# Kernel tuning notes

Hardware: AMD Instinct MI355X
Metric: run time of the kernel (lower is better)

## Reference

```python
import jax, jax.numpy as jnp
import numpy as np

B, N, C, L, H = 8, 128, 64, 3, 128  # batch, objects, channels, eq-layers, message hidden
NEG_SLOPE = 0.01  # torch leaky_relu default


def setup_inputs() -> dict:
    key = jax.random.key(0)
    ks = jax.random.split(key, 10)
    def p(k, shape, fan):
        return jax.random.normal(k, shape, dtype=jnp.float32) * np.float32(np.sqrt(2.0 / fan))
    return {
        "x": jax.random.normal(ks[0], (B, N, N, C), dtype=jnp.float32),
        "mask": jnp.ones((B, N, N, 1), dtype=jnp.float32),
        # MessageNet per eq-layer: Linear(C->H), Linear(H->H), Linear(H->C), stacked over L layers
        "msg_w1": p(ks[1], (L, H, C), C + H),
        "msg_b1": jnp.zeros((L, H), jnp.float32),
        "msg_w2": p(ks[2], (L, H, H), H + H),
        "msg_b2": jnp.zeros((L, H), jnp.float32),
        "msg_w3": p(ks[3], (L, C, H), H + C),
        "msg_b3": jnp.zeros((L, C), jnp.float32),
        # Eq2to2 params: coefs (in_dim, out_dim, 15), bias, diag_bias
        "coefs": p(ks[4], (L, C, C, 15), C + C + 15),
        "bias": jnp.zeros((L, C), jnp.float32),
        "diag_bias": jnp.zeros((L, C), jnp.float32),
    }


def leaky(x):
    return jax.nn.leaky_relu(x, NEG_SLOPE)


def eops_2_to_2(x):
    # x: (B, m, m, C) -> ops: (B, C, 15, m, m); aggregation='sum'
    t = jnp.transpose(x, (0, 3, 1, 2))            # (B, C, m, m)
    m = t.shape[-1]
    eye = jnp.eye(m, dtype=t.dtype)
    diag = jnp.diagonal(t, axis1=-2, axis2=-1)    # (B, C, m)
    sum_diag = diag.sum(-1, keepdims=True)        # (B, C, 1)
    sum_rows = t.sum(-1)                          # (B, C, m)  sum over j
    sum_cols = t.sum(-2)                          # (B, C, m)  sum over i
    sum_all = t.sum((-2, -1))[..., None]          # (B, C, 1)
    de = lambda v: v[..., :, None] * eye          # diag_embed with broadcast
    shp = t.shape
    bc = lambda a: jnp.broadcast_to(a, shp)
    ops = [
        de(diag),                                 # 1  diag -> diag
        de(sum_diag),                             # 2  trace -> diag
        de(sum_rows),                             # 3  row sums -> diag
        de(sum_cols),                             # 4  col sums -> diag
        de(sum_all),                              # 5  total sum -> diag
        bc(sum_cols[..., :, None]),               # 6  col sums broadcast over j
        bc(sum_rows[..., :, None]),               # 7  row sums broadcast over j
        bc(sum_cols[..., None, :]),               # 8  col sums broadcast over i
        bc(sum_rows[..., None, :]),               # 9  row sums broadcast over i
        t,                                        # 10 identity
        jnp.swapaxes(t, -2, -1),                  # 11 transpose
        bc(diag[..., :, None]),                   # 12 diag broadcast over j
        bc(diag[..., None, :]),                   # 13 diag broadcast over i
        bc(sum_diag[..., :, None]),               # 14 trace broadcast everywhere
        bc(sum_all[..., :, None]),                # 15 total sum broadcast everywhere
    ]
    return jnp.stack(ops, axis=2)                 # (B, C, 15, m, m)


def reference(x, mask, msg_w1, msg_b1, msg_w2, msg_b2, msg_w3, msg_b3, coefs, bias, diag_bias):
    m = x.shape[1]
    eye = jnp.eye(m, dtype=x.dtype)[None, :, :, None]  # (1, m, m, 1)
    for l in range(L):
        # MessageNet: pointwise MLP over channels, activation after each linear, then mask
        h = leaky(jnp.einsum('nijc,hc->nijh', x, msg_w1[l]) + msg_b1[l])
        h = leaky(jnp.einsum('nijc,hc->nijh', h, msg_w2[l]) + msg_b2[l])
        h = leaky(jnp.einsum('nijc,hc->nijh', h, msg_w3[l]) + msg_b3[l])
        h = h * mask
        # Eq2to2
        ops = eops_2_to_2(h)                              # (B, C, 15, m, m)
        out = jnp.einsum('dsb,ndbij->nijs', coefs[l], ops)
        out = out + bias[l][None, None, None, :] + eye * diag_bias[l][None, None, None, :]
        out = leaky(out)
        x = out * mask
    return x
```

## Files before the change

### kernel.cpp

```cpp
#include <hip/hip_runtime.h>
#include <hip/hip_bf16.h>

#define BB 8
#define NN 128
#define CC 64
#define LL 3
#define HH 128
#define NEG 0.01f
#define NPOS (BB*NN*NN)

typedef __attribute__((ext_vector_type(8))) short shortx8;
typedef __attribute__((ext_vector_type(4))) float f32x4;

#define OFF_HHI   0L
#define OFF_RS2   4194304L
#define OFF_XN    8388608L
#define OFF_RS    12582912L
#define OFF_DG    12648448L
#define OFF_RCDH  12713984L
#define OFF_RCDL  12812288L
#define OFF_U     12911616L
#define OFF_V     12977152L
#define OFF_D     13042688L
#define OFF_SB    13108224L

__device__ __forceinline__ float leaky(float v) { return v >= 0.f ? v : NEG * v; }

__device__ __forceinline__ short f2bf(float f) {
    return (short)__bfloat16_as_ushort(__float2bfloat16(f));
}
__device__ __forceinline__ float bf2f(short s) {
    unsigned u = ((unsigned)(unsigned short)s) << 16;
    return __builtin_bit_cast(float, u);
}
__device__ __forceinline__ unsigned pkf(float a, float b) {
    return (unsigned)(unsigned short)f2bf(a) | ((unsigned)(unsigned short)f2bf(b) << 16);
}
__device__ __forceinline__ shortx8 cvt8(const float* p) {
    float4 f0 = *(const float4*)p, f1 = *(const float4*)(p + 4);
    shortx8 r;
    r[0]=f2bf(f0.x); r[1]=f2bf(f0.y); r[2]=f2bf(f0.z); r[3]=f2bf(f0.w);
    r[4]=f2bf(f1.x); r[5]=f2bf(f1.y); r[6]=f2bf(f1.z); r[7]=f2bf(f1.w);
    return r;
}

__global__ void prep_kernel(const float* __restrict__ w1, const float* __restrict__ w2,
                            const float* __restrict__ w3, const float* __restrict__ coefs,
                            float* __restrict__ ws) {
    long idx = (long)blockIdx.x * 256 + threadIdx.x;
    short* sb = (short*)(ws + OFF_SB);
    if (idx < 24576) {
        sb[idx] = f2bf(w1[idx]);
    } else if (idx < 73728) {
        sb[idx] = f2bf(w2[idx - 24576]);
    } else if (idx < 98304) {
        sb[idx] = f2bf(w3[idx - 73728]);
    } else if (idx < 110592) {
        long r = idx - 98304; int l = (int)(r / 4096); int q = (int)(r % 4096);
        int s = q >> 6, d = q & 63;
        float v = coefs[(((long)l*CC + d)*CC + s)*15 + 9];
        short hi = f2bf(v);
        sb[98304 + r]  = hi;
        sb[110592 + r] = f2bf(v - bf2f(hi));
    } else if (idx < 122880) {
        long r = idx - 110592; int l = (int)(r / 4096); int q = (int)(r % 4096);
        int s = q >> 6, d = q & 63;
        float v = coefs[(((long)l*CC + d)*CC + s)*15 + 10];
        short hi = f2bf(v);
        sb[122880 + r] = hi;
        sb[135168 + r] = f2bf(v - bf2f(hi));
    } else if (idx < 233472) {
        long r = idx - 122880;
        int l = (int)(r / 36864); int q = (int)(r % 36864);
        int o = q / 192, k = q % 192;
        int wo = o >> 6, s = o & 63, wk = k >> 6, d = k & 63;
        const int sel[3][3] = {{5,6,11},{7,8,12},{3,2,0}};
        float v = coefs[(((long)l*CC + d)*CC + s)*15 + sel[wo][wk]];
        short hi = f2bf(v);
        sb[147456 + r] = hi;
        sb[258048 + r] = f2bf(v - bf2f(hi));
    }
}

__global__ __launch_bounds__(256, 5) void mlp_kernel(
    const float* __restrict__ xf, const short* __restrict__ xb,
    const float* __restrict__ mask,
    const float* __restrict__ b1, const float* __restrict__ b2, const float* __restrict__ b3,
    const short* __restrict__ wb1, const short* __restrict__ wb2, const short* __restrict__ wb3,
    short* __restrict__ hout, float* __restrict__ rowsum2, float* __restrict__ diagOut)
{
    __shared__ __align__(16) char lds[32768];
    const int t = threadIdx.x;
    const int lane = t & 63;
    const int w = t >> 6;
    const int arow = lane & 15;
    const int kgrp = lane >> 4;
    const long pos0 = (long)blockIdx.x * 64;
    const int XT = 16384;

    {
        const int row = t >> 2, q = t & 3;
        const long off = (pos0 + row)*CC + q*16;
        shortx8 v0, v1;
        if (xb) { v0 = *(const shortx8*)(xb + off); v1 = *(const shortx8*)(xb + off + 8); }
        else    { v0 = cvt8(xf + off);              v1 = cvt8(xf + off + 8); }
        const int swz = (row & 7) << 4;
        *(shortx8*)(&lds[XT + row*128 + ((q*32)      ^ swz)]) = v0;
        *(shortx8*)(&lds[XT + row*128 + ((q*32 + 16) ^ swz)]) = v1;
    }
    __syncthreads();

    {
        f32x4 acc[2][4];
        #pragma unroll
        for (int of = 0; of < 2; ++of)
            #pragma unroll
            for (int pf = 0; pf < 4; ++pf) acc[of][pf] = (f32x4){0.f,0.f,0.f,0.f};
        #pragma unroll
        for (int kk = 0; kk < 2; ++kk) {
            shortx8 bx[4];
            #pragma unroll
            for (int pf = 0; pf < 4; ++pf) {
                const int p = pf*16 + arow;
                bx[pf] = *(const shortx8*)(&lds[XT + p*128 + ((kk*64 + kgrp*16) ^ ((p & 7) << 4))]);
            }
            #pragma unroll
            for (int of = 0; of < 2; ++of) {
                const shortx8 a = *(const shortx8*)(wb1 + (long)(w*32 + of*16 + arow)*CC + kk*32 + kgrp*8);
                #pragma unroll
                for (int pf = 0; pf < 4; ++pf)
                    acc[of][pf] = __builtin_amdgcn_mfma_f32_16x16x32_bf16(a, bx[pf], acc[of][pf], 0, 0, 0);
            }
        }
        #pragma unroll
        for (int of = 0; of < 2; ++of) {
            const int o0 = w*32 + of*16 + kgrp*4;
            const float4 bv = *(const float4*)(b1 + o0);
            #pragma unroll
            for (int pf = 0; pf < 4; ++pf) {
                const int p = pf*16 + arow;
                unsigned u0 = pkf(leaky(acc[of][pf][0] + bv.x), leaky(acc[of][pf][1] + bv.y));
                unsigned u1 = pkf(leaky(acc[of][pf][2] + bv.z), leaky(acc[of][pf][3] + bv.w));
                *(uint2*)(&lds[p*256 + ((o0*2) ^ ((p & 15) << 4))]) = make_uint2(u0, u1);
            }
        }
    }
    __syncthreads();

    {
        f32x4 acc[2][4];
        #pragma unroll
        for (int of = 0; of < 2; ++of)
            #pragma unroll
            for (int pf = 0; pf < 4; ++pf) acc[of][pf] = (f32x4){0.f,0.f,0.f,0.f};
        #pragma unroll
        for (int kk = 0; kk < 4; ++kk) {
            shortx8 bx[4];
            #pragma unroll
            for (int pf = 0; pf < 4; ++pf) {
                const int p = pf*16 + arow;
                bx[pf] = *(const shortx8*)(&lds[p*256 + ((kk*64 + kgrp*16) ^ ((p & 15) << 4))]);
            }
            #pragma unroll
            for (int of = 0; of < 2; ++of) {
                const shortx8 a = *(const shortx8*)(wb2 + (long)(w*32 + of*16 + arow)*HH + kk*32 + kgrp*8);
                #pragma unroll
                for (int pf = 0; pf < 4; ++pf)
                    acc[of][pf] = __builtin_amdgcn_mfma_f32_16x16x32_bf16(a, bx[pf], acc[of][pf], 0, 0, 0);
            }
        }
        __syncthreads();
        #pragma unroll
        for (int of = 0; of < 2; ++of) {
            const int o0 = w*32 + of*16 + kgrp*4;
            const float4 bv = *(const float4*)(b2 + o0);
            #pragma unroll
            for (int pf = 0; pf < 4; ++pf) {
                const int p = pf*16 + arow;
                unsigned u0 = pkf(leaky(acc[of][pf][0] + bv.x), leaky(acc[of][pf][1] + bv.y));
                unsigned u1 = pkf(leaky(acc[of][pf][2] + bv.z), leaky(acc[of][pf][3] + bv.w));
                *(uint2*)(&lds[16384 + p*256 + ((o0*2) ^ ((p & 15) << 4))]) = make_uint2(u0, u1);
            }
        }
    }
    __syncthreads();

    {
        f32x4 acc[4];
        #pragma unroll
        for (int pf = 0; pf < 4; ++pf) acc[pf] = (f32x4){0.f,0.f,0.f,0.f};
        #pragma unroll
        for (int kk = 0; kk < 4; ++kk) {
            const shortx8 a = *(const shortx8*)(wb3 + (long)(w*16 + arow)*HH + kk*32 + kgrp*8);
            #pragma unroll
            for (int pf = 0; pf < 4; ++pf) {
                const int p = pf*16 + arow;
                const shortx8 bx = *(const shortx8*)(&lds[16384 + p*256 + ((kk*64 + kgrp*16) ^ ((p & 15) << 4))]);
                acc[pf] = __builtin_amdgcn_mfma_f32_16x16x32_bf16(a, bx, acc[pf], 0, 0, 0);
            }
        }
        const int o0 = w*16 + kgrp*4;
        const float4 bv = *(const float4*)(b3 + o0);
        const int rowIdx = (int)(pos0 >> 7);
        const int half64 = (int)(pos0 & 127);
        const int pDiag  = (rowIdx & 127) - half64;
        float rs0 = 0.f, rs1 = 0.f, rs2 = 0.f, rs3 = 0.f;
        #pragma unroll
        for (int pf = 0; pf < 4; ++pf) {
            const int p = pf*16 + arow;
            const long pos = pos0 + p;
            const float mv = mask[pos];
            float v0 = leaky(acc[pf][0] + bv.x) * mv;
            float v1 = leaky(acc[pf][1] + bv.y) * mv;
            float v2 = leaky(acc[pf][2] + bv.z) * mv;
            float v3 = leaky(acc[pf][3] + bv.w) * mv;
            rs0 += v0; rs1 += v1; rs2 += v2; rs3 += v3;
            if (p == pDiag)
                *(float4*)(diagOut + (long)rowIdx*CC + o0) = make_float4(v0, v1, v2, v3);
            *(uint2*)(hout + pos*CC + o0) = make_uint2(pkf(v0, v1), pkf(v2, v3));
        }
        #pragma unroll
        for (int m = 1; m < 16; m <<= 1) {
            rs0 += __shfl_xor(rs0, m);
            rs1 += __shfl_xor(rs1, m);
            rs2 += __shfl_xor(rs2, m);
            rs3 += __shfl_xor(rs3, m);
        }
        if (arow == 0)
            *(float4*)(rowsum2 + (long)blockIdx.x*CC + o0) = make_float4(rs0, rs1, rs2, rs3);
    }
}

__global__ __launch_bounds__(256) void colsum_kernel(const short* __restrict__ h,
                                                     const float* __restrict__ rowsum2,
                                                     const float* __restrict__ diagIn,
                                                     float* __restrict__ rowsum,
                                                     short* __restrict__ rcdh,
                                                     short* __restrict__ rcdl) {
    const int br = blockIdx.x;
    const int n = br >> 7, r = br & 127;
    const int t = threadIdx.x;
    const int c8 = (t & 7) * 8;
    const int g = t >> 3;
    __shared__ float red[32][64];

    {
        const long colbase = ((long)n*NN*NN + r) * CC;
        float s[8];
        #pragma unroll
        for (int e = 0; e < 8; ++e) s[e] = 0.f;
        for (int i = g; i < NN; i += 32) {
            const shortx8 vh = *(const shortx8*)(h + colbase + (long)i*NN*CC + c8);
            #pragma unroll
            for (int e = 0; e < 8; ++e) s[e] += bf2f(vh[e]);
        }
        #pragma unroll
        for (int e = 0; e < 8; ++e) red[g][c8 + e] = s[e];
    }
    __syncthreads();
    if (t < 64) {
        float cs = 0.f;
        #pragma unroll
        for (int k = 0; k < 32; ++k) cs += red[k][t];
        short hh = f2bf(cs);
        rcdh[(long)br*192 + t] = hh;
        rcdl[(long)br*192 + t] = f2bf(cs - bf2f(hh));
        const float rs = rowsum2[(long)(br*2)*CC + t] + rowsum2[(long)(br*2+1)*CC + t];
        rowsum[(long)br*CC + t] = rs;
        short hr = f2bf(rs);
        rcdh[(long)br*192 + 64 + t] = hr;
        rcdl[(long)br*192 + 64 + t] = f2bf(rs - bf2f(hr));
        const float dg = diagIn[(long)br*CC + t];
        short hd = f2bf(dg);
        rcdh[(long)br*192 + 128 + t] = hd;
        rcdl[(long)br*192 + 128 + t] = f2bf(dg - bf2f(hd));
    }
}

__global__ __launch_bounds__(256) void uvd_kernel(
    const short* __restrict__ rcdh, const short* __restrict__ rcdl,
    const short* __restrict__ kh, const short* __restrict__ kl,
    const float* __restrict__ rowsum, const float* __restrict__ diag,
    const float* __restrict__ coefs, int layer,
    float* __restrict__ U, float* __restrict__ V, float* __restrict__ D)
{
    __shared__ float ra[4][64], rb[4][64];
    __shared__ float ub[64], db[64];
    const int t = threadIdx.x, lane = t & 63, w = t >> 6;
    const int arow = lane & 15, kgrp = lane >> 4;
    const int r0 = blockIdx.x * 64;
    const int nb = r0 >> 7;

    {
        const int c = t & 63, g = t >> 6;
        float a = 0.f, b = 0.f;
        for (int i = g; i < NN; i += 4) {
            a += rowsum[((long)nb*NN + i)*CC + c];
            b += diag[((long)nb*NN + i)*CC + c];
        }
        ra[g][c] = a; rb[g][c] = b;
    }
    __syncthreads();
    if (t < 128) {
        const int which = t >> 6, s = t & 63;
        const float* cf = coefs + (long)layer*CC*CC*15;
        float acc = 0.f;
        for (int d = 0; d < CC; ++d) {
            const float tt = ra[0][d] + ra[1][d] + ra[2][d] + ra[3][d];
            const float tr = rb[0][d] + rb[1][d] + rb[2][d] + rb[3][d];
            const float* cds = cf + ((long)d*CC + s)*15;
            if (which == 0) acc += cds[13]*tr + cds[14]*tt;
            else            acc += cds[1]*tr + cds[4]*tt;
        }
        if (which == 0) ub[s] = acc; else db[s] = acc;
    }
    __syncthreads();

    f32x4 acc[3][4];
    #pragma unroll
    for (int o = 0; o < 3; ++o)
        #pragma unroll
        for (int pf = 0; pf < 4; ++pf) acc[o][pf] = (f32x4){0.f,0.f,0.f,0.f};
    #pragma unroll
    for (int kk = 0; kk < 6; ++kk) {
        shortx8 bh[4], bl[4];
        #pragma unroll
        for (int pf = 0; pf < 4; ++pf) {
            const long off = (long)(r0 + pf*16 + arow)*192 + kk*32 + kgrp*8;
            bh[pf] = *(const shortx8*)(rcdh + off);
            bl[pf] = *(const shortx8*)(rcdl + off);
        }
        #pragma unroll
        for (int o = 0; o < 3; ++o) {
            const long aoff = (long)((w*3 + o)*16 + arow)*192 + kk*32 + kgrp*8;
            const shortx8 ah = *(const shortx8*)(kh + aoff);
            const shortx8 al = *(const shortx8*)(kl + aoff);
            #pragma unroll
            for (int pf = 0; pf < 4; ++pf) {
                acc[o][pf] = __builtin_amdgcn_mfma_f32_16x16x32_bf16(ah, bh[pf], acc[o][pf], 0, 0, 0);
                acc[o][pf] = __builtin_amdgcn_mfma_f32_16x16x32_bf16(ah, bl[pf], acc[o][pf], 0, 0, 0);
                acc[o][pf] = __builtin_amdgcn_mfma_f32_16x16x32_bf16(al, bh[pf], acc[o][pf], 0, 0, 0);
            }
        }
    }
    #pragma unroll
    for (int o = 0; o < 3; ++o) {
        const int o16 = (w*3 + o)*16;
        const int o0 = o16 + kgrp*4;
        #pragma unroll
        for (int pf = 0; pf < 4; ++pf) {
            const long rr = r0 + pf*16 + arow;
            float4 a = make_float4(acc[o][pf][0], acc[o][pf][1], acc[o][pf][2], acc[o][pf][3]);
            if (o16 < 64) {
                a.x += ub[o0]; a.y += ub[o0+1]; a.z += ub[o0+2]; a.w += ub[o0+3];
                *(float4*)(U + rr*CC + o0) = a;
            } else if (o16 < 128) {
                *(float4*)(V + rr*CC + (o0 - 64)) = a;
            } else {
                const int q = o0 - 128;
                a.x += db[q]; a.y += db[q+1]; a.z += db[q+2]; a.w += db[q+3];
                *(float4*)(D + rr*CC + q) = a;
            }
        }
    }
}

__global__ __launch_bounds__(256, 6) void eq_kernel(
    const short* __restrict__ h, const float* __restrict__ mask,
    const short* __restrict__ c9h, const short* __restrict__ c9l,
    const short* __restrict__ c10h, const short* __restrict__ c10l,
    const float* __restrict__ U, const float* __restrict__ V, const float* __restrict__ D,
    const float* __restrict__ bias, const float* __restrict__ idbias,
    float* __restrict__ outf, short* __restrict__ outb)
{
    __shared__ __align__(16) char lds[16384];
    const int t = threadIdx.x, lane = t & 63, w = t >> 6;
    const int arow = lane & 15, kgrp = lane >> 4;
    const int n = blockIdx.y;
    const int pr = blockIdx.x;
    int it = (int)((sqrtf(8.f*pr + 1.f) - 1.f)*0.5f);
    while ((it+1)*(it+2)/2 <= pr) ++it;
    while (it*(it+1)/2 > pr) --it;
    const int jt = pr - it*(it+1)/2;
    const int i0 = it*8, j0 = jt*8;
    const int s0 = w*16;

    shortx8 A9h[2], A9l[2], A10h[2], A10l[2];
    #pragma unroll
    for (int kk = 0; kk < 2; ++kk) {
        const long co = (long)(s0 + arow)*CC + kk*32 + kgrp*8;
        A9h[kk]  = *(const shortx8*)(c9h  + co);
        A9l[kk]  = *(const shortx8*)(c9l  + co);
        A10h[kk] = *(const shortx8*)(c10h + co);
        A10l[kk] = *(const shortx8*)(c10l + co);
    }

    {
        const int row = t >> 2, q = t & 3;
        const long posA = ((long)n*NN + i0 + (row >> 3))*NN + (j0 + (row & 7));
        const long posM = ((long)n*NN + j0 + (row & 7))*NN + (i0 + (row >> 3));
        const short* sA = h + posA*CC + q*16;
        const short* sM = h + posM*CC + q*16;
        shortx8 v0 = *(const shortx8*)(sA);
        shortx8 v1 = *(const shortx8*)(sA + 8);
        shortx8 v4 = *(const shortx8*)(sM);
        shortx8 v5 = *(const shortx8*)(sM + 8);
        const int swz = (row & 7) << 4;
        const int d0 = row*128 + ((q*32) ^ swz);
        const int d1 = row*128 + ((q*32 + 16) ^ swz);
        *(shortx8*)(&lds[d0]) = v0;          *(shortx8*)(&lds[d1]) = v1;
        *(shortx8*)(&lds[8192 + d0]) = v4;   *(shortx8*)(&lds[8192 + d1]) = v5;
    }
    __syncthreads();

    f32x4 accA[4], accM[4];
    #pragma unroll
    for (int pf = 0; pf < 4; ++pf) { accA[pf] = (f32x4){0.f,0.f,0.f,0.f}; accM[pf] = (f32x4){0.f,0.f,0.f,0.f}; }

    #pragma unroll
    for (int kk = 0; kk < 2; ++kk) {
        #pragma unroll
        for (int pf = 0; pf < 4; ++pf) {
            const int p = pf*16 + arow;
            const int off = (kk*64 + kgrp*16) ^ ((p & 7) << 4);
            const shortx8 Ah = *(const shortx8*)(&lds[p*128 + off]);
            const shortx8 Mh = *(const shortx8*)(&lds[8192 + p*128 + off]);
            accA[pf] = __builtin_amdgcn_mfma_f32_16x16x32_bf16(A9h[kk],  Ah, accA[pf], 0, 0, 0);
            accA[pf] = __builtin_amdgcn_mfma_f32_16x16x32_bf16(A9l[kk],  Ah, accA[pf], 0, 0, 0);
            accA[pf] = __builtin_amdgcn_mfma_f32_16x16x32_bf16(A10h[kk], Mh, accA[pf], 0, 0, 0);
            accA[pf] = __builtin_amdgcn_mfma_f32_16x16x32_bf16(A10l[kk], Mh, accA[pf], 0, 0, 0);
            accM[pf] = __builtin_amdgcn_mfma_f32_16x16x32_bf16(A9h[kk],  Mh, accM[pf], 0, 0, 0);
            accM[pf] = __builtin_amdgcn_mfma_f32_16x16x32_bf16(A9l[kk],  Mh, accM[pf], 0, 0, 0);
            accM[pf] = __builtin_amdgcn_mfma_f32_16x16x32_bf16(A10h[kk], Ah, accM[pf], 0, 0, 0);
            accM[pf] = __builtin_amdgcn_mfma_f32_16x16x32_bf16(A10l[kk], Ah, accM[pf], 0, 0, 0);
        }
    }

    const int sc = s0 + kgrp*4;
    const float4 bv = *(const float4*)(bias + sc);
    #pragma unroll
    for (int pf = 0; pf < 4; ++pf) {
        const int p = pf*16 + arow;
        {
            const int pi = i0 + (p >> 3), pj = j0 + (p & 7);
            const long pix = ((long)n*NN + pi)*NN + pj;
            const float4 u4 = *(const float4*)(U + ((long)n*NN + pi)*CC + sc);
            const float4 v4 = *(const float4*)(V + ((long)n*NN + pj)*CC + sc);
            float vv[4];
            vv[0] = accA[pf][0] + u4.x + v4.x + bv.x;
            vv[1] = accA[pf][1] + u4.y + v4.y + bv.y;
            vv[2] = accA[pf][2] + u4.z + v4.z + bv.z;
            vv[3] = accA[pf][3] + u4.w + v4.w + bv.w;
            if (it == jt && pi == pj) {
                const float4 d4  = *(const float4*)(D + ((long)n*NN + pi)*CC + sc);
                const float4 db4 = *(const float4*)(idbias + sc);
                vv[0] += d4.x + db4.x; vv[1] += d4.y + db4.y;
                vv[2] += d4.z + db4.z; vv[3] += d4.w + db4.w;
            }
            const float mv = mask[pix];
            #pragma unroll
            for (int r = 0; r < 4; ++r) vv[r] = leaky(vv[r]) * mv;
            if (outf) *(float4*)(outf + pix*CC + sc) = make_float4(vv[0], vv[1], vv[2], vv[3]);
            else      *(uint2*)(outb + pix*CC + sc) = make_uint2(pkf(vv[0], vv[1]), pkf(vv[2], vv[3]));
        }
        if (it != jt) {
            const int pi = j0 + (p & 7), pj = i0 + (p >> 3);
            const long pix = ((long)n*NN + pi)*NN + pj;
            const float4 u4 = *(const float4*)(U + ((long)n*NN + pi)*CC + sc);
            const float4 v4 = *(const float4*)(V + ((long)n*NN + pj)*CC + sc);
            float vv[4];
            vv[0] = accM[pf][0] + u4.x + v4.x + bv.x;
            vv[1] = accM[pf][1] + u4.y + v4.y + bv.y;
            vv[2] = accM[pf][2] + u4.z + v4.z + bv.z;
            vv[3] = accM[pf][3] + u4.w + v4.w + bv.w;
            const float mv = mask[pix];
            #pragma unroll
            for (int r = 0; r < 4; ++r) vv[r] = leaky(vv[r]) * mv;
            if (outf) *(float4*)(outf + pix*CC + sc) = make_float4(vv[0], vv[1], vv[2], vv[3]);
            else      *(uint2*)(outb + pix*CC + sc) = make_uint2(pkf(vv[0], vv[1]), pkf(vv[2], vv[3]));
        }
    }
}

extern "C" void kernel_launch(void* const* d_in, const int* in_sizes, int n_in,
                              void* d_out, int out_size, void* d_ws, size_t ws_size,
                              hipStream_t stream) {
    const float* x     = (const float*)d_in[0];
    const float* mask  = (const float*)d_in[1];
    const float* w1    = (const float*)d_in[2];
    const float* b1    = (const float*)d_in[3];
    const float* w2    = (const float*)d_in[4];
    const float* b2    = (const float*)d_in[5];
    const float* w3    = (const float*)d_in[6];
    const float* b3    = (const float*)d_in[7];
    const float* coefs = (const float*)d_in[8];
    const float* bias  = (const float*)d_in[9];
    const float* idb   = (const float*)d_in[10];
    float* out = (float*)d_out;
    float* ws  = (float*)d_ws;

    short* hh      = (short*)(ws + OFF_HHI);
    float* rowsum2 = ws + OFF_RS2;
    short* xn      = (short*)(ws + OFF_XN);
    float* rowsum  = ws + OFF_RS;
    float* diag    = ws + OFF_DG;
    short* rcdh    = (short*)(ws + OFF_RCDH);
    short* rcdl    = (short*)(ws + OFF_RCDL);
    float* U       = ws + OFF_U;
    float* V       = ws + OFF_V;
    float* D       = ws + OFF_D;
    short* sb      = (short*)(ws + OFF_SB);

    prep_kernel<<<912, 256, 0, stream>>>(w1, w2, w3, coefs, ws);

    for (int l = 0; l < LL; ++l) {
        mlp_kernel<<<NPOS/64, 256, 0, stream>>>(
            (l == 0) ? x : nullptr, (l == 0) ? nullptr : xn, mask,
            b1 + l*HH, b2 + l*HH, b3 + l*CC,
            sb + (long)l*HH*CC, sb + 24576 + (long)l*HH*HH, sb + 73728 + (long)l*CC*HH,
            hh, rowsum2, diag);
        colsum_kernel<<<BB*NN, 256, 0, stream>>>(hh, rowsum2, diag, rowsum, rcdh, rcdl);
        uvd_kernel<<<16, 256, 0, stream>>>(rcdh, rcdl,
            sb + 147456 + (long)l*36864, sb + 258048 + (long)l*36864,
            rowsum, diag, coefs, l, U, V, D);
        eq_kernel<<<dim3(136, BB), 256, 0, stream>>>(
            hh, mask,
            sb + 98304 + (long)l*CC*CC, sb + 110592 + (long)l*CC*CC,
            sb + 122880 + (long)l*CC*CC, sb + 135168 + (long)l*CC*CC,
            U, V, D, bias + l*CC, idb + l*CC,
            (l == LL-1) ? out : nullptr, (l == LL-1) ? nullptr : xn);
    }
}
```

Measured before the change: 236.1 us.

## Make each wave own 16 positions in MLP kernel, removing block barriers

The MLP kernel is restructured so each wave computes all output channels for its own 16 positions, instead of splitting output channels across waves over a 64-position tile. Inputs are loaded directly from global memory into registers, and each wave uses its own LDS region for the hidden activations. This removes all __syncthreads and the shared input staging. The cost is that every wave now reads the full weight matrices, and row sums are written per wave, so colsum_kernel reduces 8 partials instead of 2. The occupancy hint is lowered from 5 to 4 blocks per SM.

```diff
diff --git a/kernel.cpp b/kernel.cpp
--- a/kernel.cpp
+++ b/kernel.cpp
@@ -82,7 +82,7 @@
     }
 }
 
-__global__ __launch_bounds__(256, 5) void mlp_kernel(
+__global__ __launch_bounds__(256, 4) void mlp_kernel(
     const float* __restrict__ xf, const short* __restrict__ xb,
     const float* __restrict__ mask,
     const float* __restrict__ b1, const float* __restrict__ b2, const float* __restrict__ b3,
@@ -96,138 +96,91 @@
     const int arow = lane & 15;
     const int kgrp = lane >> 4;
     const long pos0 = (long)blockIdx.x * 64;
-    const int XT = 16384;
+    const long pos  = pos0 + w*16 + arow;
+    const int h1b = w*4096;
+    const int h2b = 16384 + w*4096;
+    const int swz = arow << 4;
+
+    shortx8 bx[2];
+    #pragma unroll
+    for (int kk = 0; kk < 2; ++kk) {
+        const long off = pos*CC + kk*32 + kgrp*8;
+        bx[kk] = xb ? *(const shortx8*)(xb + off) : cvt8(xf + off);
+    }
+
+    #pragma unroll
+    for (int of = 0; of < 8; ++of) {
+        f32x4 acc = (f32x4){0.f,0.f,0.f,0.f};
+        #pragma unroll
+        for (int kk = 0; kk < 2; ++kk) {
+            const shortx8 a = *(const shortx8*)(wb1 + (long)(of*16 + arow)*CC + kk*32 + kgrp*8);
+            acc = __builtin_amdgcn_mfma_f32_16x16x32_bf16(a, bx[kk], acc, 0, 0, 0);
+        }
+        const int o0 = of*16 + kgrp*4;
+        const float4 bv = *(const float4*)(b1 + o0);
+        unsigned u0 = pkf(leaky(acc[0] + bv.x), leaky(acc[1] + bv.y));
+        unsigned u1 = pkf(leaky(acc[2] + bv.z), leaky(acc[3] + bv.w));
+        *(uint2*)(&lds[h1b + arow*256 + ((o0*2) ^ swz)]) = make_uint2(u0, u1);
+    }
 
     {
-        const int row = t >> 2, q = t & 3;
-        const long off = (pos0 + row)*CC + q*16;
-        shortx8 v0, v1;
-        if (xb) { v0 = *(const shortx8*)(xb + off); v1 = *(const shortx8*)(xb + off + 8); }
-        else    { v0 = cvt8(xf + off);              v1 = cvt8(xf + off + 8); }
-        const int swz = (row & 7) << 4;
-        *(shortx8*)(&lds[XT + row*128 + ((q*32)      ^ swz)]) = v0;
-        *(shortx8*)(&lds[XT + row*128 + ((q*32 + 16) ^ swz)]) = v1;
-    }
-    __syncthreads();
+        shortx8 b2x[4];
+        #pragma unroll
+        for (int kk = 0; kk < 4; ++kk)
+            b2x[kk] = *(const shortx8*)(&lds[h1b + arow*256 + ((kk*64 + kgrp*16) ^ swz)]);
+        #pragma unroll
+        for (int of = 0; of < 8; ++of) {
+            f32x4 acc = (f32x4){0.f,0.f,0.f,0.f};
+            #pragma unroll
+            for (int kk = 0; kk < 4; ++kk) {
+                const shortx8 a = *(const shortx8*)(wb2 + (long)(of*16 + arow)*HH + kk*32 + kgrp*8);
+                acc = __builtin_amdgcn_mfma_f32_16x16x32_bf16(a, b2x[kk], acc, 0, 0, 0);
+            }
+            const int o0 = of*16 + kgrp*4;
+            const float4 bv = *(const float4*)(b2 + o0);
+            unsigned u0 = pkf(leaky(acc[0] + bv.x), leaky(acc[1] + bv.y));
+            unsigned u1 = pkf(leaky(acc[2] + bv.z), leaky(acc[3] + bv.w));
+            *(uint2*)(&lds[h2b + arow*256 + ((o0*2) ^ swz)]) = make_uint2(u0, u1);
+        }
+    }
 
     {
-        f32x4 acc[2][4];
-        #pragma unroll
-        for (int of = 0; of < 2; ++of)
-            #pragma unroll
-            for (int pf = 0; pf < 4; ++pf) acc[of][pf] = (f32x4){0.f,0.f,0.f,0.f};
-        #pragma unroll
-        for (int kk = 0; kk < 2; ++kk) {
-            shortx8 bx[4];
-            #pragma unroll
-            for (int pf = 0; pf < 4; ++pf) {
-                const int p = pf*16 + arow;
-                bx[pf] = *(const shortx8*)(&lds[XT + p*128 + ((kk*64 + kgrp*16) ^ ((p & 7) << 4))]);
-            }
-            #pragma unroll
-            for (int of = 0; of < 2; ++of) {
-                const shortx8 a = *(const shortx8*)(wb1 + (long)(w*32 + of*16 + arow)*CC + kk*32 + kgrp*8);
-                #pragma unroll
-                for (int pf = 0; pf < 4; ++pf)
-                    acc[of][pf] = __builtin_amdgcn_mfma_f32_16x16x32_bf16(a, bx[pf], acc[of][pf], 0, 0, 0);
-            }
-        }
-        #pragma unroll
-        for (int of = 0; of < 2; ++of) {
-            const int o0 = w*32 + of*16 + kgrp*4;
-            const float4 bv = *(const float4*)(b1 + o0);
-            #pragma unroll
-            for (int pf = 0; pf < 4; ++pf) {
-                const int p = pf*16 + arow;
-                unsigned u0 = pkf(leaky(acc[of][pf][0] + bv.x), leaky(acc[of][pf][1] + bv.y));
-                unsigned u1 = pkf(leaky(acc[of][pf][2] + bv.z), leaky(acc[of][pf][3] + bv.w));
-                *(uint2*)(&lds[p*256 + ((o0*2) ^ ((p & 15) << 4))]) = make_uint2(u0, u1);
-            }
-        }
-    }
-    __syncthreads();
-
-    {
-        f32x4 acc[2][4];
-        #pragma unroll
-        for (int of = 0; of < 2; ++of)
-            #pragma unroll
-            for (int pf = 0; pf < 4; ++pf) acc[of][pf] = (f32x4){0.f,0.f,0.f,0.f};
-        #pragma unroll
-        for (int kk = 0; kk < 4; ++kk) {
-            shortx8 bx[4];
-            #pragma unroll
-            for (int pf = 0; pf < 4; ++pf) {
-                const int p = pf*16 + arow;
-                bx[pf] = *(const shortx8*)(&lds[p*256 + ((kk*64 + kgrp*16) ^ ((p & 15) << 4))]);
-            }
-            #pragma unroll
-            for (int of = 0; of < 2; ++of) {
-                const shortx8 a = *(const shortx8*)(wb2 + (long)(w*32 + of*16 + arow)*HH + kk*32 + kgrp*8);
-                #pragma unroll
-                for (int pf = 0; pf < 4; ++pf)
-                    acc[of][pf] = __builtin_amdgcn_mfma_f32_16x16x32_bf16(a, bx[pf], acc[of][pf], 0, 0, 0);
-            }
-        }
-        __syncthreads();
-        #pragma unroll
-        for (int of = 0; of < 2; ++of) {
-            const int o0 = w*32 + of*16 + kgrp*4;
-            const float4 bv = *(const float4*)(b2 + o0);
-            #pragma unroll
-            for (int pf = 0; pf < 4; ++pf) {
-                const int p = pf*16 + arow;
-                unsigned u0 = pkf(leaky(acc[of][pf][0] + bv.x), leaky(acc[of][pf][1] + bv.y));
-                unsigned u1 = pkf(leaky(acc[of][pf][2] + bv.z), leaky(acc[of][pf][3] + bv.w));
-                *(uint2*)(&lds[16384 + p*256 + ((o0*2) ^ ((p & 15) << 4))]) = make_uint2(u0, u1);
-            }
-        }
-    }
-    __syncthreads();
-
-    {
-        f32x4 acc[4];
-        #pragma unroll
-        for (int pf = 0; pf < 4; ++pf) acc[pf] = (f32x4){0.f,0.f,0.f,0.f};
-        #pragma unroll
-        for (int kk = 0; kk < 4; ++kk) {
-            const shortx8 a = *(const shortx8*)(wb3 + (long)(w*16 + arow)*HH + kk*32 + kgrp*8);
-            #pragma unroll
-            for (int pf = 0; pf < 4; ++pf) {
-                const int p = pf*16 + arow;
-                const shortx8 bx = *(const shortx8*)(&lds[16384 + p*256 + ((kk*64 + kgrp*16) ^ ((p & 15) << 4))]);
-                acc[pf] = __builtin_amdgcn_mfma_f32_16x16x32_bf16(a, bx, acc[pf], 0, 0, 0);
-            }
-        }
-        const int o0 = w*16 + kgrp*4;
-        const float4 bv = *(const float4*)(b3 + o0);
-        const int rowIdx = (int)(pos0 >> 7);
-        const int half64 = (int)(pos0 & 127);
-        const int pDiag  = (rowIdx & 127) - half64;
-        float rs0 = 0.f, rs1 = 0.f, rs2 = 0.f, rs3 = 0.f;
-        #pragma unroll
-        for (int pf = 0; pf < 4; ++pf) {
-            const int p = pf*16 + arow;
-            const long pos = pos0 + p;
-            const float mv = mask[pos];
-            float v0 = leaky(acc[pf][0] + bv.x) * mv;
-            float v1 = leaky(acc[pf][1] + bv.y) * mv;
-            float v2 = leaky(acc[pf][2] + bv.z) * mv;
-            float v3 = leaky(acc[pf][3] + bv.w) * mv;
-            rs0 += v0; rs1 += v1; rs2 += v2; rs3 += v3;
-            if (p == pDiag)
-                *(float4*)(diagOut + (long)rowIdx*CC + o0) = make_float4(v0, v1, v2, v3);
+        shortx8 b3x[4];
+        #pragma unroll
+        for (int kk = 0; kk < 4; ++kk)
+            b3x[kk] = *(const shortx8*)(&lds[h2b + arow*256 + ((kk*64 + kgrp*16) ^ swz)]);
+        const float mv = mask[pos];
+        const bool isDiag = ((int)(pos & 127)) == ((int)((pos >> 7) & 127));
+        const long rowIdx = pos >> 7;
+        const long slot = (long)blockIdx.x*4 + w;
+        #pragma unroll
+        for (int of = 0; of < 4; ++of) {
+            f32x4 acc = (f32x4){0.f,0.f,0.f,0.f};
+            #pragma unroll
+            for (int kk = 0; kk < 4; ++kk) {
+                const shortx8 a = *(const shortx8*)(wb3 + (long)(of*16 + arow)*HH + kk*32 + kgrp*8);
+                acc = __builtin_amdgcn_mfma_f32_16x16x32_bf16(a, b3x[kk], acc, 0, 0, 0);
+            }
+            const int o0 = of*16 + kgrp*4;
+            const float4 bv = *(const float4*)(b3 + o0);
+            float v0 = leaky(acc[0] + bv.x) * mv;
+            float v1 = leaky(acc[1] + bv.y) * mv;
+            float v2 = leaky(acc[2] + bv.z) * mv;
+            float v3 = leaky(acc[3] + bv.w) * mv;
             *(uint2*)(hout + pos*CC + o0) = make_uint2(pkf(v0, v1), pkf(v2, v3));
-        }
-        #pragma unroll
-        for (int m = 1; m < 16; m <<= 1) {
-            rs0 += __shfl_xor(rs0, m);
-            rs1 += __shfl_xor(rs1, m);
-            rs2 += __shfl_xor(rs2, m);
-            rs3 += __shfl_xor(rs3, m);
-        }
-        if (arow == 0)
-            *(float4*)(rowsum2 + (long)blockIdx.x*CC + o0) = make_float4(rs0, rs1, rs2, rs3);
+            if (isDiag)
+                *(float4*)(diagOut + rowIdx*CC + o0) = make_float4(v0, v1, v2, v3);
+            float rs0 = v0, rs1 = v1, rs2 = v2, rs3 = v3;
+            #pragma unroll
+            for (int m = 1; m < 16; m <<= 1) {
+                rs0 += __shfl_xor(rs0, m);
+                rs1 += __shfl_xor(rs1, m);
+                rs2 += __shfl_xor(rs2, m);
+                rs3 += __shfl_xor(rs3, m);
+            }
+            if (arow == 0)
+                *(float4*)(rowsum2 + slot*CC + o0) = make_float4(rs0, rs1, rs2, rs3);
+        }
     }
 }
 
@@ -265,7 +218,9 @@
         short hh = f2bf(cs);
         rcdh[(long)br*192 + t] = hh;
         rcdl[(long)br*192 + t] = f2bf(cs - bf2f(hh));
-        const float rs = rowsum2[(long)(br*2)*CC + t] + rowsum2[(long)(br*2+1)*CC + t];
+        float rs = 0.f;
+        #pragma unroll
+        for (int q = 0; q < 8; ++q) rs += rowsum2[((long)br*8 + q)*CC + t];
         rowsum[(long)br*CC + t] = rs;
         short hr = f2bf(rs);
         rcdh[(long)br*192 + 64 + t] = hr;
```

Result: slower. 362.6 us (+53.6%).

## Fuse column-sum and U/V/D projection into one kernel per row

Applied to the files above, without the earlier changes.

Merges colsum_kernel and the small 16-block uvd_kernel into one cuvd_kernel launched per (batch,row). Each block computes its column sums, then projects column, row and diagonal sums through the coefficients with scalar fp32 FMAs instead of split-bf16 MFMA. This drops one launch per layer, the rcd staging buffers and the prep work for the projection weights. In exchange, every block recomputes the batch-wide trace and total sums (the ub/db terms) by reading 128 rows of rowsum2 and diag, and reads coefs with a strided scalar access pattern.

```diff
diff --git a/kernel.cpp b/kernel.cpp
--- a/kernel.cpp
+++ b/kernel.cpp
@@ -15,10 +15,7 @@
 #define OFF_HHI   0L
 #define OFF_RS2   4194304L
 #define OFF_XN    8388608L
-#define OFF_RS    12582912L
 #define OFF_DG    12648448L
-#define OFF_RCDH  12713984L
-#define OFF_RCDL  12812288L
 #define OFF_U     12911616L
 #define OFF_V     12977152L
 #define OFF_D     13042688L
@@ -69,16 +66,6 @@
         short hi = f2bf(v);
         sb[122880 + r] = hi;
         sb[135168 + r] = f2bf(v - bf2f(hi));
-    } else if (idx < 233472) {
-        long r = idx - 122880;
-        int l = (int)(r / 36864); int q = (int)(r % 36864);
-        int o = q / 192, k = q % 192;
-        int wo = o >> 6, s = o & 63, wk = k >> 6, d = k & 63;
-        const int sel[3][3] = {{5,6,11},{7,8,12},{3,2,0}};
-        float v = coefs[(((long)l*CC + d)*CC + s)*15 + sel[wo][wk]];
-        short hi = f2bf(v);
-        sb[147456 + r] = hi;
-        sb[258048 + r] = f2bf(v - bf2f(hi));
     }
 }
 
@@ -231,20 +218,21 @@
     }
 }
 
-__global__ __launch_bounds__(256) void colsum_kernel(const short* __restrict__ h,
-                                                     const float* __restrict__ rowsum2,
-                                                     const float* __restrict__ diagIn,
-                                                     float* __restrict__ rowsum,
-                                                     short* __restrict__ rcdh,
-                                                     short* __restrict__ rcdl) {
+__global__ __launch_bounds__(256) void cuvd_kernel(
+    const short* __restrict__ h,
+    const float* __restrict__ rowsum2, const float* __restrict__ diagIn,
+    const float* __restrict__ coefs, int layer,
+    float* __restrict__ U, float* __restrict__ V, float* __restrict__ D)
+{
     const int br = blockIdx.x;
     const int n = br >> 7, r = br & 127;
     const int t = threadIdx.x;
-    const int c8 = (t & 7) * 8;
-    const int g = t >> 3;
     __shared__ float red[32][64];
-
-    {
+    __shared__ float csS[64], rsS[64], dgS[64];
+    __shared__ float ubS[64], dbS[64];
+
+    {
+        const int c8 = (t & 7) * 8, g = t >> 3;
         const long colbase = ((long)n*NN*NN + r) * CC;
         float s[8];
         #pragma unroll
@@ -262,43 +250,21 @@
         float cs = 0.f;
         #pragma unroll
         for (int k = 0; k < 32; ++k) cs += red[k][t];
-        short hh = f2bf(cs);
-        rcdh[(long)br*192 + t] = hh;
-        rcdl[(long)br*192 + t] = f2bf(cs - bf2f(hh));
-        const float rs = rowsum2[(long)(br*2)*CC + t] + rowsum2[(long)(br*2+1)*CC + t];
-        rowsum[(long)br*CC + t] = rs;
-        short hr = f2bf(rs);
-        rcdh[(long)br*192 + 64 + t] = hr;
-        rcdl[(long)br*192 + 64 + t] = f2bf(rs - bf2f(hr));
-        const float dg = diagIn[(long)br*CC + t];
-        short hd = f2bf(dg);
-        rcdh[(long)br*192 + 128 + t] = hd;
-        rcdl[(long)br*192 + 128 + t] = f2bf(dg - bf2f(hd));
-    }
-}
-
-__global__ __launch_bounds__(256) void uvd_kernel(
-    const short* __restrict__ rcdh, const short* __restrict__ rcdl,
-    const short* __restrict__ kh, const short* __restrict__ kl,
-    const float* __restrict__ rowsum, const float* __restrict__ diag,
-    const float* __restrict__ coefs, int layer,
-    float* __restrict__ U, float* __restrict__ V, float* __restrict__ D)
-{
-    __shared__ float ra[4][64], rb[4][64];
-    __shared__ float ub[64], db[64];
-    const int t = threadIdx.x, lane = t & 63, w = t >> 6;
-    const int arow = lane & 15, kgrp = lane >> 4;
-    const int r0 = blockIdx.x * 64;
-    const int nb = r0 >> 7;
-
+        csS[t] = cs;
+        rsS[t] = rowsum2[(long)(br*2)*CC + t] + rowsum2[(long)(br*2+1)*CC + t];
+        dgS[t] = diagIn[(long)br*CC + t];
+    }
+    __syncthreads();
     {
         const int c = t & 63, g = t >> 6;
         float a = 0.f, b = 0.f;
         for (int i = g; i < NN; i += 4) {
-            a += rowsum[((long)nb*NN + i)*CC + c];
-            b += diag[((long)nb*NN + i)*CC + c];
-        }
-        ra[g][c] = a; rb[g][c] = b;
+            const long bri = (long)(n*NN + i);
+            a += rowsum2[bri*2*CC + c] + rowsum2[(bri*2+1)*CC + c];
+            b += diagIn[bri*CC + c];
+        }
+        red[g][c] = a;
+        red[4 + g][c] = b;
     }
     __syncthreads();
     if (t < 128) {
@@ -306,62 +272,29 @@
         const float* cf = coefs + (long)layer*CC*CC*15;
         float acc = 0.f;
         for (int d = 0; d < CC; ++d) {
-            const float tt = ra[0][d] + ra[1][d] + ra[2][d] + ra[3][d];
-            const float tr = rb[0][d] + rb[1][d] + rb[2][d] + rb[3][d];
+            const float tt = red[0][d] + red[1][d] + red[2][d] + red[3][d];
+            const float tr = red[4][d] + red[5][d] + red[6][d] + red[7][d];
             const float* cds = cf + ((long)d*CC + s)*15;
             if (which == 0) acc += cds[13]*tr + cds[14]*tt;
             else            acc += cds[1]*tr + cds[4]*tt;
         }
-        if (which == 0) ub[s] = acc; else db[s] = acc;
-    }
-    __syncthreads();
-
-    f32x4 acc[3][4];
-    #pragma unroll
-    for (int o = 0; o < 3; ++o)
-        #pragma unroll
-        for (int pf = 0; pf < 4; ++pf) acc[o][pf] = (f32x4){0.f,0.f,0.f,0.f};
-    #pragma unroll
-    for (int kk = 0; kk < 6; ++kk) {
-        shortx8 bh[4], bl[4];
-        #pragma unroll
-        for (int pf = 0; pf < 4; ++pf) {
-            const long off = (long)(r0 + pf*16 + arow)*192 + kk*32 + kgrp*8;
-            bh[pf] = *(const shortx8*)(rcdh + off);
-            bl[pf] = *(const shortx8*)(rcdl + off);
-        }
-        #pragma unroll
-        for (int o = 0; o < 3; ++o) {
-            const long aoff = (long)((w*3 + o)*16 + arow)*192 + kk*32 + kgrp*8;
-            const shortx8 ah = *(const shortx8*)(kh + aoff);
-            const shortx8 al = *(const shortx8*)(kl + aoff);
-            #pragma unroll
-            for (int pf = 0; pf < 4; ++pf) {
-                acc[o][pf] = __builtin_amdgcn_mfma_f32_16x16x32_bf16(ah, bh[pf], acc[o][pf], 0, 0, 0);
-                acc[o][pf] = __builtin_amdgcn_mfma_f32_16x16x32_bf16(ah, bl[pf], acc[o][pf], 0, 0, 0);
-                acc[o][pf] = __builtin_amdgcn_mfma_f32_16x16x32_bf16(al, bh[pf], acc[o][pf], 0, 0, 0);
-            }
-        }
-    }
-    #pragma unroll
-    for (int o = 0; o < 3; ++o) {
-        const int o16 = (w*3 + o)*16;
-        const int o0 = o16 + kgrp*4;
-        #pragma unroll
-        for (int pf = 0; pf < 4; ++pf) {
-            const long rr = r0 + pf*16 + arow;
-            float4 a = make_float4(acc[o][pf][0], acc[o][pf][1], acc[o][pf][2], acc[o][pf][3]);
-            if (o16 < 64) {
-                a.x += ub[o0]; a.y += ub[o0+1]; a.z += ub[o0+2]; a.w += ub[o0+3];
-                *(float4*)(U + rr*CC + o0) = a;
-            } else if (o16 < 128) {
-                *(float4*)(V + rr*CC + (o0 - 64)) = a;
-            } else {
-                const int q = o0 - 128;
-                a.x += db[q]; a.y += db[q+1]; a.z += db[q+2]; a.w += db[q+3];
-                *(float4*)(D + rr*CC + q) = a;
-            }
-        }
+        if (which == 0) ubS[s] = acc; else dbS[s] = acc;
+    }
+    __syncthreads();
+    if (t < 192) {
+        const int which = t >> 6, s = t & 63;
+        const float* cf = coefs + (long)layer*CC*CC*15;
+        float acc = 0.f;
+        for (int d = 0; d < CC; ++d) {
+            const float* cds = cf + ((long)d*CC + s)*15;
+            const float cs = csS[d], rs = rsS[d], dg = dgS[d];
+            if (which == 0)      acc += cds[5]*cs + cds[6]*rs + cds[11]*dg;
+            else if (which == 1) acc += cds[7]*cs + cds[8]*rs + cds[12]*dg;
+            else                 acc += cds[3]*cs + cds[2]*rs + cds[0]*dg;
+        }
+        if (which == 0)      U[(long)br*CC + s] = acc + ubS[s];
+        else if (which == 1) V[(long)br*CC + s] = acc;
+        else                 D[(long)br*CC + s] = acc + dbS[s];
     }
 }
 
@@ -502,16 +435,13 @@
     short* hh      = (short*)(ws + OFF_HHI);
     float* rowsum2 = ws + OFF_RS2;
     short* xn      = (short*)(ws + OFF_XN);
-    float* rowsum  = ws + OFF_RS;
     float* diag    = ws + OFF_DG;
-    short* rcdh    = (short*)(ws + OFF_RCDH);
-    short* rcdl    = (short*)(ws + OFF_RCDL);
     float* U       = ws + OFF_U;
     float* V       = ws + OFF_V;
     float* D       = ws + OFF_D;
     short* sb      = (short*)(ws + OFF_SB);
 
-    prep_kernel<<<912, 256, 0, stream>>>(w1, w2, w3, coefs, ws);
+    prep_kernel<<<480, 256, 0, stream>>>(w1, w2, w3, coefs, ws);
 
     for (int l = 0; l < LL; ++l) {
         mlp_kernel<<<NPOS/64, 256, 0, stream>>>(
@@ -519,10 +449,7 @@
             b1 + l*HH, b2 + l*HH, b3 + l*CC,
             sb + (long)l*HH*CC, sb + 24576 + (long)l*HH*HH, sb + 73728 + (long)l*CC*HH,
             hh, rowsum2, diag);
-        colsum_kernel<<<BB*NN, 256, 0, stream>>>(hh, rowsum2, diag, rowsum, rcdh, rcdl);
-        uvd_kernel<<<16, 256, 0, stream>>>(rcdh, rcdl,
-            sb + 147456 + (long)l*36864, sb + 258048 + (long)l*36864,
-            rowsum, diag, coefs, l, U, V, D);
+        cuvd_kernel<<<BB*NN, 256, 0, stream>>>(hh, rowsum2, diag, coefs, l, U, V, D);
         eq_kernel<<<dim3(136, BB), 256, 0, stream>>>(
             hh, mask,
             sb + 98304 + (long)l*CC*CC, sb + 110592 + (long)l*CC*CC,
```

New measurement: 274.0 us. 16.1% more time.
